# Kernel tuning notes

Measured on AMD Instinct MI355X. Metric: run time of the kernel, lower is better.

## Reference

```python
import jax, jax.numpy as jnp
import numpy as np

B, D, H, FPL, L, LOG2_T = 65536, 768, 512, 4, 16, 19
T = 2 ** LOG2_T
BASE_RES, FINEST_RES = 16, 512
PRIMES = jnp.array([1, 2654435761, 805459861], dtype=jnp.uint32)


def setup_inputs() -> dict:
    key = jax.random.key(0)
    ks = jax.random.split(key, 8)
    t = jax.random.uniform(ks[0], (B,), dtype=jnp.float32)
    x = jax.random.normal(ks[1], (B, D), dtype=jnp.float32)
    cond = jax.random.uniform(ks[2], (B, 2), dtype=jnp.float32)
    # one embedding table per level, Instant-NGP init U(-1e-4, 1e-4)
    tables = jax.random.uniform(ks[3], (L, T, FPL), dtype=jnp.float32,
                                minval=-1e-4, maxval=1e-4)
    in_dim = D + L * FPL  # 832

    def lin(k, fan_in, fan_out):
        return jax.random.normal(k, (fan_in, fan_out), dtype=jnp.float32) / np.sqrt(fan_in).astype(np.float32)

    W0, b0 = lin(ks[4], in_dim, H), jnp.zeros((H,), jnp.float32)
    W1, b1 = lin(ks[5], H, H), jnp.zeros((H,), jnp.float32)
    W2, b2 = lin(ks[6], H, H), jnp.zeros((H,), jnp.float32)
    W3, b3 = lin(ks[7], H, D), jnp.zeros((D,), jnp.float32)
    return dict(t=t, x=x, cond=cond, tables=tables,
                W0=W0, b0=b0, W1=W1, b1=b1, W2=W2, b2=b2, W3=W3, b3=b3)


def hash_encode(coords, tables):
    """coords: [B,3] in [0,1]; tables: [L,T,F] -> [B, L*F]."""
    Ln, Tn, Fn = tables.shape
    growth = np.exp((np.log(FINEST_RES) - np.log(BASE_RES)) / (Ln - 1))
    scales = jnp.asarray(np.floor(BASE_RES * growth ** np.arange(Ln)),
                         dtype=coords.dtype)                      # [L]
    xf = coords[:, None, :] * scales[None, :, None]               # [B,L,3]
    xl = jnp.floor(xf)
    w = xf - xl                                                   # [B,L,3] trilinear frac
    xi = xl.astype(jnp.uint32)
    # 8 cube-corner offsets
    offs = jnp.asarray(np.stack(np.meshgrid([0, 1], [0, 1], [0, 1],
                                            indexing='ij'), -1).reshape(8, 3),
                       dtype=jnp.uint32)                          # [8,3]
    corners = xi[:, :, None, :] + offs[None, None]                # [B,L,8,3]
    h = corners * PRIMES                                          # uint32 wraparound hash
    idx = (h[..., 0] ^ h[..., 1] ^ h[..., 2]) & jnp.uint32(Tn - 1)  # [B,L,8]
    feats = tables[jnp.arange(Ln)[None, :, None], idx]            # [B,L,8,F] gather
    offs_f = offs.astype(coords.dtype)
    wc = jnp.prod(jnp.where(offs_f[None, None] == 1,
                            w[:, :, None, :], 1 - w[:, :, None, :]), axis=-1)  # [B,L,8]
    out = jnp.einsum('blc,blcf->blf', wc, feats)                  # [B,L,F]
    return out.reshape(out.shape[0], Ln * Fn)


def reference(t, x, cond, tables, W0, b0, W1, b1, W2, b2, W3, b3):
    tcol = t[:, None] if t.ndim == 1 else t
    params3 = jnp.concatenate([cond, tcol], axis=-1)   # [B,3]
    enc = hash_encode(params3, tables)                  # [B,64]
    h = jnp.concatenate([x, enc], axis=-1)              # [B,832]
    h = jax.nn.silu(h @ W0 + b0)
    h = jax.nn.silu(h @ W1 + b1)
    h = jax.nn.silu(h @ W2 + b2)
    return h @ W3 + b3                                  # [B,768]
```

## Files before the change

### kernel.cpp

```cpp
#include <hip/hip_runtime.h>
#include <hip/hip_bf16.h>
#include <math.h>


#define T_SIZE 524288
#define T_MASK (T_SIZE - 1)

typedef _Float16 f16;
typedef _Float16 f16x8 __attribute__((ext_vector_type(8)));
typedef _Float16 f16x4 __attribute__((ext_vector_type(4)));
typedef float f32x4 __attribute__((ext_vector_type(4)));

struct Scales { float s[16]; };

#define GLD16(gsrc, ldst) __builtin_amdgcn_global_load_lds( \
    (const __attribute__((address_space(1))) void*)(gsrc),  \
    (__attribute__((address_space(3))) void*)(ldst), 16, 0, 0)

__global__ void wfrag(const float* __restrict__ W, f16* __restrict__ Wf, int K, int N) {
  int tid = blockIdx.x * 256 + threadIdx.x;
  int lane = tid & 63, frag = tid >> 6;
  int KS = K >> 5;
  int nblk = frag / KS, ks = frag - nblk * KS;
  if (nblk * 16 >= N) return;
  int n = nblk * 16 + (lane & 15);
  int kb = ks * 32 + (lane >> 4) * 8;
  f16x8 v;
#pragma unroll
  for (int j = 0; j < 8; ++j) v[j] = (f16)W[(size_t)(kb + j) * N + n];
  *(f16x8*)(Wf + (size_t)frag * 512 + lane * 8) = v;
}

__device__ __forceinline__ float silu_f(float v) {
  return v * __builtin_amdgcn_rcpf(1.f + __expf(-v));
}

__device__ __forceinline__ f16x8 cvt8(f32x4 a, f32x4 b) {
  return (f16x8){ (f16)a.x, (f16)a.y, (f16)a.z, (f16)a.w,
                  (f16)b.x, (f16)b.y, (f16)b.z, (f16)b.w };
}

__global__ __launch_bounds__(256) void prep(
    const float* __restrict__ x, const float* __restrict__ t,
    const float* __restrict__ cond, const float* __restrict__ tables,
    f16* __restrict__ H0, Scales scl) {
  const int row = blockIdx.x * 32 + (threadIdx.x >> 3);
  const int c8 = threadIdx.x & 7;
  const float* xr = x + (size_t)row * 768;
  f16* hr = H0 + (size_t)row * 832;

  {
    float c0 = cond[2 * row], c1 = cond[2 * row + 1], c2 = t[row];
    unsigned idx[2][8];
    float    wcw[2][8];
#pragma unroll
    for (int d = 0; d < 2; ++d) {
      int l = c8 * 2 + d;
      float s = scl.s[l];
      float xf0 = c0 * s, xf1 = c1 * s, xf2 = c2 * s;
      float xl0 = floorf(xf0), xl1 = floorf(xf1), xl2 = floorf(xf2);
      float w0 = xf0 - xl0, w1 = xf1 - xl1, w2 = xf2 - xl2;
      unsigned xi0 = (unsigned)xl0, xi1 = (unsigned)xl1, xi2 = (unsigned)xl2;
      unsigned h0 = xi0, h1 = xi1 * 2654435761u, h2 = xi2 * 805459861u;
      unsigned g0 = xi0 + 1u, g1 = (xi1 + 1u) * 2654435761u, g2 = (xi2 + 1u) * 805459861u;
#pragma unroll
      for (int c = 0; c < 8; ++c) {
        unsigned ax = (c >> 2) & 1u, ay = (c >> 1) & 1u, az = c & 1u;
        unsigned hh = (ax ? g0 : h0) ^ (ay ? g1 : h1) ^ (az ? g2 : h2);
        idx[d][c] = hh & T_MASK;
        wcw[d][c] = (ax ? w0 : 1.f - w0) * (ay ? w1 : 1.f - w1) * (az ? w2 : 1.f - w2);
      }
    }
    const f32x4* tl0 = (const f32x4*)tables + (size_t)(c8 * 2) * T_SIZE;
    f32x4 fv[2][8];
#pragma unroll
    for (int d = 0; d < 2; ++d)
#pragma unroll
      for (int c = 0; c < 8; ++c)
        fv[d][c] = tl0[(size_t)d * T_SIZE + idx[d][c]];
    f16x8 er;
#pragma unroll
    for (int d = 0; d < 2; ++d) {
      float a0 = 0.f, a1 = 0.f, a2 = 0.f, a3 = 0.f;
#pragma unroll
      for (int c = 0; c < 8; ++c) {
        a0 += wcw[d][c] * fv[d][c].x; a1 += wcw[d][c] * fv[d][c].y;
        a2 += wcw[d][c] * fv[d][c].z; a3 += wcw[d][c] * fv[d][c].w;
      }
      er[d * 4 + 0] = (f16)a0; er[d * 4 + 1] = (f16)a1;
      er[d * 4 + 2] = (f16)a2; er[d * 4 + 3] = (f16)a3;
    }
    *(f16x8*)(hr + 768 + c8 * 8) = er;
  }

#pragma unroll
  for (int j = 0; j < 12; ++j) {
    int col = j * 64 + c8 * 8;
    f32x4 a = __builtin_nontemporal_load((const f32x4*)(xr + col));
    f32x4 b = __builtin_nontemporal_load((const f32x4*)(xr + col + 4));
    *(f16x8*)(hr + col) = cvt8(a, b);
  }
}

template<int NF, int KSTEPS>
__device__ __forceinline__ void kloop_dp(
    const f16* __restrict__ actS, const f16* __restrict__ Wf, int fragRow0,
    int l16, int lhi, int lane, f32x4 (&acc)[4][4]) {
#pragma unroll
  for (int mi = 0; mi < 4; ++mi)
#pragma unroll
    for (int ni = 0; ni < NF; ++ni) acc[mi][ni] = (f32x4){0.f, 0.f, 0.f, 0.f};

  f16x8 bfU[NF], bfV[NF];
  const f16* wbase = Wf + ((size_t)fragRow0 * KSTEPS) * 512 + lane * 8;
#pragma unroll
  for (int ni = 0; ni < NF; ++ni)
    bfU[ni] = *(const f16x8*)(wbase + (size_t)(ni * KSTEPS + 0) * 512);
#pragma unroll
  for (int ni = 0; ni < NF; ++ni)
    bfV[ni] = *(const f16x8*)(wbase + (size_t)(ni * KSTEPS + 1) * 512);

#pragma unroll 1
  for (int ks = 0; ks < KSTEPS; ks += 2) {
    f16x8 af[4];
#pragma unroll
    for (int mi = 0; mi < 4; ++mi) {
      int r = mi * 16 + l16;
      af[mi] = *(const f16x8*)(actS + r * 512 + ((ks * 32 + lhi * 8) ^ ((r & 7) << 3)));
    }
#pragma unroll
    for (int mi = 0; mi < 4; ++mi)
#pragma unroll
      for (int ni = 0; ni < NF; ++ni)
        acc[mi][ni] = __builtin_amdgcn_mfma_f32_16x16x32_f16(bfU[ni], af[mi], acc[mi][ni], 0, 0, 0);
    if (ks + 2 < KSTEPS) {
#pragma unroll
      for (int ni = 0; ni < NF; ++ni)
        bfU[ni] = *(const f16x8*)(wbase + (size_t)(ni * KSTEPS + ks + 2) * 512);
    }
#pragma unroll
    for (int mi = 0; mi < 4; ++mi) {
      int r = mi * 16 + l16;
      af[mi] = *(const f16x8*)(actS + r * 512 + (((ks + 1) * 32 + lhi * 8) ^ ((r & 7) << 3)));
    }
#pragma unroll
    for (int mi = 0; mi < 4; ++mi)
#pragma unroll
      for (int ni = 0; ni < NF; ++ni)
        acc[mi][ni] = __builtin_amdgcn_mfma_f32_16x16x32_f16(bfV[ni], af[mi], acc[mi][ni], 0, 0, 0);
    if (ks + 3 < KSTEPS) {
#pragma unroll
      for (int ni = 0; ni < NF; ++ni)
        bfV[ni] = *(const f16x8*)(wbase + (size_t)(ni * KSTEPS + ks + 3) * 512);
    }
  }
}

__global__ __launch_bounds__(1024, 4) void fused_mlp(
    const f16* __restrict__ H0,
    const f16* __restrict__ Wf0, const f16* __restrict__ Wf1,
    const f16* __restrict__ Wf2, const f16* __restrict__ Wf3,
    const float* __restrict__ b0, const float* __restrict__ b1,
    const float* __restrict__ b2, const float* __restrict__ b3,
    float* __restrict__ outp) {
  __shared__ f16 act[128 * 512];
  f16* stg = act;

  const int tid = threadIdx.x;
  const int wave = tid >> 6, lane = tid & 63;
  const int l16 = lane & 15, lhi = lane >> 4;
  const int wr = wave >> 3, wc = wave & 7;
  const int rowBase = blockIdx.x * 128;
  const int r = tid >> 3, c8 = tid & 7;

  const f16* h0r = H0 + (size_t)(rowBase + r) * 832 + (size_t)((c8 ^ (r & 7)) * 8);
  f16* ldsA = stg + wave * 512;
  f16* ldsB = stg + 8192 + wave * 512;

  f32x4 acc[4][4];
#pragma unroll
  for (int mi = 0; mi < 4; ++mi)
#pragma unroll
    for (int ni = 0; ni < 4; ++ni) acc[mi][ni] = (f32x4){0.f, 0.f, 0.f, 0.f};

  {
    GLD16(h0r, ldsA);
    __syncthreads();
#pragma unroll 1
    for (int ks = 0; ks < 13; ++ks) {
      if (ks < 12) GLD16(h0r + (ks + 1) * 64, (ks & 1) ? ldsA : ldsB);
      f16x8 bf[2][4];
#pragma unroll
      for (int kk = 0; kk < 2; ++kk)
#pragma unroll
        for (int ni = 0; ni < 4; ++ni)
          bf[kk][ni] = *(const f16x8*)(Wf0 + (size_t)((wc * 4 + ni) * 26 + ks * 2 + kk) * 512 + lane * 8);
      const f16* rb = stg + (ks & 1) * 8192 + wr * 4096;
#pragma unroll
      for (int kk = 0; kk < 2; ++kk)
#pragma unroll
        for (int mi = 0; mi < 4; ++mi) {
          int r2 = mi * 16 + l16;
          f16x8 af = *(const f16x8*)(rb + r2 * 64 + (((kk * 4 + lhi) ^ (r2 & 7)) << 3));
#pragma unroll
          for (int ni = 0; ni < 4; ++ni)
            acc[mi][ni] = __builtin_amdgcn_mfma_f32_16x16x32_f16(bf[kk][ni], af, acc[mi][ni], 0, 0, 0);
        }
      __syncthreads();
    }
  }

  auto epi_act = [&](const float* __restrict__ bias) {
    __syncthreads();
#pragma unroll
    for (int mi = 0; mi < 4; ++mi) {
      const int row = wr * 64 + mi * 16 + l16;
#pragma unroll
      for (int ni = 0; ni < 4; ++ni) {
        const int col = wc * 64 + ni * 16 + lhi * 4;
        float4 bv = *(const float4*)(bias + col);
        f16x4 o;
        o[0] = (f16)silu_f(acc[mi][ni][0] + bv.x);
        o[1] = (f16)silu_f(acc[mi][ni][1] + bv.y);
        o[2] = (f16)silu_f(acc[mi][ni][2] + bv.z);
        o[3] = (f16)silu_f(acc[mi][ni][3] + bv.w);
        *(f16x4*)(act + row * 512 + (col ^ ((row & 7) << 3))) = o;
      }
    }
    __syncthreads();
  };
  epi_act(b0);

  const f16* actW = act + wr * 64 * 512;

  kloop_dp<4, 16>(actW, Wf1, wc * 4, l16, lhi, lane, acc); epi_act(b1);
  kloop_dp<4, 16>(actW, Wf2, wc * 4, l16, lhi, lane, acc); epi_act(b2);

  kloop_dp<4, 16>(actW, Wf3, wc * 4, l16, lhi, lane, acc);
#pragma unroll
  for (int mi = 0; mi < 4; ++mi) {
    const size_t row = (size_t)(rowBase + wr * 64 + mi * 16 + l16);
#pragma unroll
    for (int ni = 0; ni < 4; ++ni) {
      const int col = wc * 64 + ni * 16 + lhi * 4;
      float4 bv = *(const float4*)(b3 + col);
      f32x4 o = { acc[mi][ni][0] + bv.x, acc[mi][ni][1] + bv.y,
                  acc[mi][ni][2] + bv.z, acc[mi][ni][3] + bv.w };
      __builtin_nontemporal_store(o, (f32x4*)(outp + row * 768 + col));
    }
  }

  kloop_dp<2, 16>(actW, Wf3, 32 + wc * 2, l16, lhi, lane, acc);
#pragma unroll
  for (int mi = 0; mi < 4; ++mi) {
    const size_t row = (size_t)(rowBase + wr * 64 + mi * 16 + l16);
#pragma unroll
    for (int ni = 0; ni < 2; ++ni) {
      const int col = 512 + wc * 32 + ni * 16 + lhi * 4;
      float4 bv = *(const float4*)(b3 + col);
      f32x4 o = { acc[mi][ni][0] + bv.x, acc[mi][ni][1] + bv.y,
                  acc[mi][ni][2] + bv.z, acc[mi][ni][3] + bv.w };
      __builtin_nontemporal_store(o, (f32x4*)(outp + row * 768 + col));
    }
  }
}

extern "C" void kernel_launch(void* const* d_in, const int* in_sizes, int n_in,
                              void* d_out, int out_size, void* d_ws, size_t ws_size,
                              hipStream_t stream) {
  const float* t    = (const float*)d_in[0];
  const float* x    = (const float*)d_in[1];
  const float* cond = (const float*)d_in[2];
  const float* tab  = (const float*)d_in[3];
  const float* W0   = (const float*)d_in[4];
  const float* b0   = (const float*)d_in[5];
  const float* W1   = (const float*)d_in[6];
  const float* b1   = (const float*)d_in[7];
  const float* W2   = (const float*)d_in[8];
  const float* b2   = (const float*)d_in[9];
  const float* W3   = (const float*)d_in[10];
  const float* b3   = (const float*)d_in[11];
  float* out = (float*)d_out;
  (void)in_sizes; (void)n_in; (void)out_size; (void)ws_size;

  char* ws = (char*)d_ws;
  f16* Wf0 = (f16*)(ws + 0);
  f16* Wf1 = (f16*)(ws + 851968);
  f16* Wf2 = (f16*)(ws + 1376256);
  f16* Wf3 = (f16*)(ws + 1900544);
  f16* H0  = (f16*)(ws + 2686976);

  wfrag<<<dim3(208), 256, 0, stream>>>(W0, Wf0, 832, 512);
  wfrag<<<dim3(128), 256, 0, stream>>>(W1, Wf1, 512, 512);
  wfrag<<<dim3(128), 256, 0, stream>>>(W2, Wf2, 512, 512);
  wfrag<<<dim3(192), 256, 0, stream>>>(W3, Wf3, 512, 768);

  Scales sc;
  {
    double growth = exp((log(512.0) - log(16.0)) / 15.0);
    for (int l = 0; l < 16; ++l) sc.s[l] = (float)floor(16.0 * pow(growth, (double)l));
  }

  prep<<<dim3(2048), 256, 0, stream>>>(x, t, cond, tab, H0, sc);

  fused_mlp<<<dim3(512), 1024, 0, stream>>>(H0, Wf0, Wf1, Wf2, Wf3,
                                            b0, b1, b2, b3, out);
}
```

Before: 348.3 us.

## Fuse hash-encoding and x conversion into the MLP kernel, drop H0 buffer

Removes the separate prep kernel that wrote an f16 [B,832] H0 buffer. The fused kernel now computes the hash encoding per block into a small LDS array and streams fp32 x directly from global memory into LDS with global_load_lds, converting to f16 while loading MFMA fragments. This avoids a full write and reread of H0 plus one kernel launch. In exchange it doubles the LDS staging bytes for the layer-0 input, adds conversion work in the inner loop, and places the gather latency at the start of every MLP block.

```diff
diff --git a/kernel.cpp b/kernel.cpp
--- a/kernel.cpp
+++ b/kernel.cpp
@@ -40,16 +40,81 @@
                   (f16)b.x, (f16)b.y, (f16)b.z, (f16)b.w };
 }
 
-__global__ __launch_bounds__(256) void prep(
+template<int NF, int KSTEPS>
+__device__ __forceinline__ void kloop_dp(
+    const f16* __restrict__ actS, const f16* __restrict__ Wf, int fragRow0,
+    int l16, int lhi, int lane, f32x4 (&acc)[4][4]) {
+#pragma unroll
+  for (int mi = 0; mi < 4; ++mi)
+#pragma unroll
+    for (int ni = 0; ni < NF; ++ni) acc[mi][ni] = (f32x4){0.f, 0.f, 0.f, 0.f};
+
+  f16x8 bfU[NF], bfV[NF];
+  const f16* wbase = Wf + ((size_t)fragRow0 * KSTEPS) * 512 + lane * 8;
+#pragma unroll
+  for (int ni = 0; ni < NF; ++ni)
+    bfU[ni] = *(const f16x8*)(wbase + (size_t)(ni * KSTEPS + 0) * 512);
+#pragma unroll
+  for (int ni = 0; ni < NF; ++ni)
+    bfV[ni] = *(const f16x8*)(wbase + (size_t)(ni * KSTEPS + 1) * 512);
+
+#pragma unroll 1
+  for (int ks = 0; ks < KSTEPS; ks += 2) {
+    f16x8 af[4];
+#pragma unroll
+    for (int mi = 0; mi < 4; ++mi) {
+      int r = mi * 16 + l16;
+      af[mi] = *(const f16x8*)(actS + r * 512 + ((ks * 32 + lhi * 8) ^ ((r & 7) << 3)));
+    }
+#pragma unroll
+    for (int mi = 0; mi < 4; ++mi)
+#pragma unroll
+      for (int ni = 0; ni < NF; ++ni)
+        acc[mi][ni] = __builtin_amdgcn_mfma_f32_16x16x32_f16(bfU[ni], af[mi], acc[mi][ni], 0, 0, 0);
+    if (ks + 2 < KSTEPS) {
+#pragma unroll
+      for (int ni = 0; ni < NF; ++ni)
+        bfU[ni] = *(const f16x8*)(wbase + (size_t)(ni * KSTEPS + ks + 2) * 512);
+    }
+#pragma unroll
+    for (int mi = 0; mi < 4; ++mi) {
+      int r = mi * 16 + l16;
+      af[mi] = *(const f16x8*)(actS + r * 512 + (((ks + 1) * 32 + lhi * 8) ^ ((r & 7) << 3)));
+    }
+#pragma unroll
+    for (int mi = 0; mi < 4; ++mi)
+#pragma unroll
+      for (int ni = 0; ni < NF; ++ni)
+        acc[mi][ni] = __builtin_amdgcn_mfma_f32_16x16x32_f16(bfV[ni], af[mi], acc[mi][ni], 0, 0, 0);
+    if (ks + 3 < KSTEPS) {
+#pragma unroll
+      for (int ni = 0; ni < NF; ++ni)
+        bfV[ni] = *(const f16x8*)(wbase + (size_t)(ni * KSTEPS + ks + 3) * 512);
+    }
+  }
+}
+
+__global__ __launch_bounds__(1024, 4) void fused_mlp(
     const float* __restrict__ x, const float* __restrict__ t,
     const float* __restrict__ cond, const float* __restrict__ tables,
-    f16* __restrict__ H0, Scales scl) {
-  const int row = blockIdx.x * 32 + (threadIdx.x >> 3);
-  const int c8 = threadIdx.x & 7;
-  const float* xr = x + (size_t)row * 768;
-  f16* hr = H0 + (size_t)row * 832;
+    const f16* __restrict__ Wf0, const f16* __restrict__ Wf1,
+    const f16* __restrict__ Wf2, const f16* __restrict__ Wf3,
+    const float* __restrict__ b0, const float* __restrict__ b1,
+    const float* __restrict__ b2, const float* __restrict__ b3,
+    float* __restrict__ outp, Scales scl) {
+  __shared__ f16 act[128 * 512];
+  __shared__ f16 encs[128 * 64];
+  char* stg = (char*)act;
+
+  const int tid = threadIdx.x;
+  const int wave = tid >> 6, lane = tid & 63;
+  const int l16 = lane & 15, lhi = lane >> 4;
+  const int wr = wave >> 3, wc = wave & 7;
+  const int rowBase = blockIdx.x * 128;
 
   {
+    const int sr = tid >> 3, c8 = tid & 7;
+    int row = rowBase + sr;
     float c0 = cond[2 * row], c1 = cond[2 * row + 1], c2 = t[row];
     unsigned idx[2][8];
     float    wcw[2][8];
@@ -90,122 +155,67 @@
       er[d * 4 + 0] = (f16)a0; er[d * 4 + 1] = (f16)a1;
       er[d * 4 + 2] = (f16)a2; er[d * 4 + 3] = (f16)a3;
     }
-    *(f16x8*)(hr + 768 + c8 * 8) = er;
-  }
-
-#pragma unroll
-  for (int j = 0; j < 12; ++j) {
-    int col = j * 64 + c8 * 8;
-    f32x4 a = __builtin_nontemporal_load((const f32x4*)(xr + col));
-    f32x4 b = __builtin_nontemporal_load((const f32x4*)(xr + col + 4));
-    *(f16x8*)(hr + col) = cvt8(a, b);
-  }
-}
-
-template<int NF, int KSTEPS>
-__device__ __forceinline__ void kloop_dp(
-    const f16* __restrict__ actS, const f16* __restrict__ Wf, int fragRow0,
-    int l16, int lhi, int lane, f32x4 (&acc)[4][4]) {
+    *(f16x8*)(encs + sr * 64 + ((c8 ^ (sr & 7)) * 8)) = er;
+  }
+
+  f32x4 acc[4][4];
 #pragma unroll
   for (int mi = 0; mi < 4; ++mi)
 #pragma unroll
-    for (int ni = 0; ni < NF; ++ni) acc[mi][ni] = (f32x4){0.f, 0.f, 0.f, 0.f};
-
-  f16x8 bfU[NF], bfV[NF];
-  const f16* wbase = Wf + ((size_t)fragRow0 * KSTEPS) * 512 + lane * 8;
-#pragma unroll
-  for (int ni = 0; ni < NF; ++ni)
-    bfU[ni] = *(const f16x8*)(wbase + (size_t)(ni * KSTEPS + 0) * 512);
-#pragma unroll
-  for (int ni = 0; ni < NF; ++ni)
-    bfV[ni] = *(const f16x8*)(wbase + (size_t)(ni * KSTEPS + 1) * 512);
+    for (int ni = 0; ni < 4; ++ni) acc[mi][ni] = (f32x4){0.f, 0.f, 0.f, 0.f};
+
+  {
+    const int srow = wave * 4 + lhi;
+    const int gch = l16 ^ (srow & 15);
+    const float* xs0 = x + (size_t)(rowBase + srow) * 768 + gch * 4;
+    const float* xs1 = x + (size_t)(rowBase + 64 + srow) * 768 + gch * 4;
+
+    GLD16(xs0, stg + wave * 1024);
+    GLD16(xs1, stg + 16384 + wave * 1024);
+    __syncthreads();
 
 #pragma unroll 1
-  for (int ks = 0; ks < KSTEPS; ks += 2) {
-    f16x8 af[4];
-#pragma unroll
-    for (int mi = 0; mi < 4; ++mi) {
-      int r = mi * 16 + l16;
-      af[mi] = *(const f16x8*)(actS + r * 512 + ((ks * 32 + lhi * 8) ^ ((r & 7) << 3)));
-    }
-#pragma unroll
-    for (int mi = 0; mi < 4; ++mi)
-#pragma unroll
-      for (int ni = 0; ni < NF; ++ni)
-        acc[mi][ni] = __builtin_amdgcn_mfma_f32_16x16x32_f16(bfU[ni], af[mi], acc[mi][ni], 0, 0, 0);
-    if (ks + 2 < KSTEPS) {
-#pragma unroll
-      for (int ni = 0; ni < NF; ++ni)
-        bfU[ni] = *(const f16x8*)(wbase + (size_t)(ni * KSTEPS + ks + 2) * 512);
-    }
-#pragma unroll
-    for (int mi = 0; mi < 4; ++mi) {
-      int r = mi * 16 + l16;
-      af[mi] = *(const f16x8*)(actS + r * 512 + (((ks + 1) * 32 + lhi * 8) ^ ((r & 7) << 3)));
-    }
-#pragma unroll
-    for (int mi = 0; mi < 4; ++mi)
-#pragma unroll
-      for (int ni = 0; ni < NF; ++ni)
-        acc[mi][ni] = __builtin_amdgcn_mfma_f32_16x16x32_f16(bfV[ni], af[mi], acc[mi][ni], 0, 0, 0);
-    if (ks + 3 < KSTEPS) {
-#pragma unroll
-      for (int ni = 0; ni < NF; ++ni)
-        bfV[ni] = *(const f16x8*)(wbase + (size_t)(ni * KSTEPS + ks + 3) * 512);
-    }
-  }
-}
-
-__global__ __launch_bounds__(1024, 4) void fused_mlp(
-    const f16* __restrict__ H0,
-    const f16* __restrict__ Wf0, const f16* __restrict__ Wf1,
-    const f16* __restrict__ Wf2, const f16* __restrict__ Wf3,
-    const float* __restrict__ b0, const float* __restrict__ b1,
-    const float* __restrict__ b2, const float* __restrict__ b3,
-    float* __restrict__ outp) {
-  __shared__ f16 act[128 * 512];
-  f16* stg = act;
-
-  const int tid = threadIdx.x;
-  const int wave = tid >> 6, lane = tid & 63;
-  const int l16 = lane & 15, lhi = lane >> 4;
-  const int wr = wave >> 3, wc = wave & 7;
-  const int rowBase = blockIdx.x * 128;
-  const int r = tid >> 3, c8 = tid & 7;
-
-  const f16* h0r = H0 + (size_t)(rowBase + r) * 832 + (size_t)((c8 ^ (r & 7)) * 8);
-  f16* ldsA = stg + wave * 512;
-  f16* ldsB = stg + 8192 + wave * 512;
-
-  f32x4 acc[4][4];
-#pragma unroll
-  for (int mi = 0; mi < 4; ++mi)
-#pragma unroll
-    for (int ni = 0; ni < 4; ++ni) acc[mi][ni] = (f32x4){0.f, 0.f, 0.f, 0.f};
-
-  {
-    GLD16(h0r, ldsA);
-    __syncthreads();
-#pragma unroll 1
-    for (int ks = 0; ks < 13; ++ks) {
-      if (ks < 12) GLD16(h0r + (ks + 1) * 64, (ks & 1) ? ldsA : ldsB);
+    for (int s = 0; s < 13; ++s) {
+      if (s < 11) {
+        char* d = stg + ((s + 1) & 1) * 32768 + wave * 1024;
+        GLD16(xs0 + (s + 1) * 64, d);
+        GLD16(xs1 + (s + 1) * 64, d + 16384);
+      }
       f16x8 bf[2][4];
 #pragma unroll
       for (int kk = 0; kk < 2; ++kk)
 #pragma unroll
         for (int ni = 0; ni < 4; ++ni)
-          bf[kk][ni] = *(const f16x8*)(Wf0 + (size_t)((wc * 4 + ni) * 26 + ks * 2 + kk) * 512 + lane * 8);
-      const f16* rb = stg + (ks & 1) * 8192 + wr * 4096;
-#pragma unroll
-      for (int kk = 0; kk < 2; ++kk)
-#pragma unroll
-        for (int mi = 0; mi < 4; ++mi) {
-          int r2 = mi * 16 + l16;
-          f16x8 af = *(const f16x8*)(rb + r2 * 64 + (((kk * 4 + lhi) ^ (r2 & 7)) << 3));
-#pragma unroll
-          for (int ni = 0; ni < 4; ++ni)
-            acc[mi][ni] = __builtin_amdgcn_mfma_f32_16x16x32_f16(bf[kk][ni], af, acc[mi][ni], 0, 0, 0);
-        }
+          bf[kk][ni] = *(const f16x8*)(Wf0 + (size_t)((wc * 4 + ni) * 26 + 2 * s + kk) * 512 + lane * 8);
+
+      if (s < 12) {
+        const char* rb = stg + (s & 1) * 32768;
+#pragma unroll
+        for (int kk = 0; kk < 2; ++kk)
+#pragma unroll
+          for (int mi = 0; mi < 4; ++mi) {
+            int r = wr * 64 + mi * 16 + l16;
+            const char* rowb = rb + r * 256;
+            int c0i = (kk * 8 + lhi * 2) ^ l16;
+            f32x4 a = *(const f32x4*)(rowb + c0i * 16);
+            f32x4 b = *(const f32x4*)(rowb + (c0i ^ 1) * 16);
+            f16x8 af = cvt8(a, b);
+#pragma unroll
+            for (int ni = 0; ni < 4; ++ni)
+              acc[mi][ni] = __builtin_amdgcn_mfma_f32_16x16x32_f16(bf[kk][ni], af, acc[mi][ni], 0, 0, 0);
+          }
+      } else {
+#pragma unroll
+        for (int kk = 0; kk < 2; ++kk)
+#pragma unroll
+          for (int mi = 0; mi < 4; ++mi) {
+            int r = wr * 64 + mi * 16 + l16;
+            f16x8 af = *(const f16x8*)(encs + r * 64 + (((kk * 4 + lhi) ^ (r & 7)) * 8));
+#pragma unroll
+            for (int ni = 0; ni < 4; ++ni)
+              acc[mi][ni] = __builtin_amdgcn_mfma_f32_16x16x32_f16(bf[kk][ni], af, acc[mi][ni], 0, 0, 0);
+          }
+      }
       __syncthreads();
     }
   }
@@ -288,7 +298,6 @@
   f16* Wf1 = (f16*)(ws + 851968);
   f16* Wf2 = (f16*)(ws + 1376256);
   f16* Wf3 = (f16*)(ws + 1900544);
-  f16* H0  = (f16*)(ws + 2686976);
 
   wfrag<<<dim3(208), 256, 0, stream>>>(W0, Wf0, 832, 512);
   wfrag<<<dim3(128), 256, 0, stream>>>(W1, Wf1, 512, 512);
@@ -301,8 +310,6 @@
     for (int l = 0; l < 16; ++l) sc.s[l] = (float)floor(16.0 * pow(growth, (double)l));
   }
 
-  prep<<<dim3(2048), 256, 0, stream>>>(x, t, cond, tab, H0, sc);
-
-  fused_mlp<<<dim3(512), 1024, 0, stream>>>(H0, Wf0, Wf1, Wf2, Wf3,
-                                            b0, b1, b2, b3, out);
-}
+  fused_mlp<<<dim3(512), 1024, 0, stream>>>(x, t, cond, tab, Wf0, Wf1, Wf2, Wf3,
+                                            b0, b1, b2, b3, out, sc);
+}
```

Result: slower. 844.0 us (+142.3%).
